# Kernel tuning notes

Hardware: AMD Instinct MI355X
Metric: run time of the kernel (lower is better)

## Reference

```python
import jax, jax.numpy as jnp
import numpy as np

B, S, L, H, N_ITEMS = 16, 20, 64, 768, 50000  # sessions, max items/session, tokens/item, hidden, catalog
T = S * L
TEMP = 0.05       # config.temp
PAD_POS = 50      # pad item position id (see torch code)
EPS = 1e-8        # torch CosineSimilarity eps


def setup_inputs() -> dict:
    key = jax.random.key(0)
    k1, k2, k3, k4 = jax.random.split(key, 4)
    hidden = jax.random.normal(k1, (B, T, H), jnp.float32)
    emb = jax.random.normal(k2, (N_ITEMS, H), jnp.float32)
    # item position ids: each item's L tokens share position 1..S; padded items -> 50
    pos = np.tile(np.repeat(np.arange(1, S + 1), L)[None, :], (B, 1))  # [B,T]
    sess_len = np.asarray(jax.random.randint(k3, (B,), S // 2, S + 1))  # items per session
    item_idx = np.repeat(np.arange(S), L)[None, :]                      # [1,T]
    pos = np.where(item_idx < sess_len[:, None], pos, PAD_POS).astype(np.int32)
    attn = (pos != PAD_POS).astype(np.int32)
    attrs = np.asarray(jax.random.randint(k4, (B, T), 0, 4)).astype(np.int32)
    return {
        "hidden_states": hidden,
        "item_embedding": emb,
        "attention_mask": jnp.asarray(attn),
        "item_position_ids": jnp.asarray(pos),
        "attr_type_ids": jnp.asarray(attrs),
    }


def reference(hidden_states, item_embedding, attention_mask, item_position_ids, attr_type_ids):
    # --- RecformerPooler (pooler_type='item'): nan-mean pool tokens per item ---
    item_ids = jnp.arange(1, S + 1, dtype=item_position_ids.dtype)
    mask = item_position_ids[:, None, :] == item_ids[None, :, None]      # [B,S,T]
    counts = mask.sum(-1)                                                # [B,S]
    valid = counts > 0                                                   # items present in session
    maskf = mask.astype(hidden_states.dtype)
    pooled = jnp.einsum('bst,bth->bsh', maskf, hidden_states)
    pooled = pooled / jnp.maximum(counts, 1)[..., None].astype(hidden_states.dtype)
    # (torch produces NaN rows for invalid items; we carry `valid` instead)

    # --- Similarity: cosine / temp vs full item catalog ---
    pn = jnp.maximum(jnp.linalg.norm(pooled, axis=-1, keepdims=True), EPS)
    en = jnp.maximum(jnp.linalg.norm(item_embedding, axis=-1, keepdims=True), EPS)
    sim = jnp.einsum('bsh,nh->bns', pooled / pn, item_embedding / en) / TEMP  # [B,N,S]

    # --- reduce_session('maxsim'): NaN -> -inf, max over session items ---
    sim = jnp.where(valid[:, None, :], sim, -jnp.inf)
    scores = sim.max(axis=-1)  # [B, N]; trailing mean over attr dim (size 1) is identity
    return scores
```

## Files before the change

### kernel.cpp

```cpp
#include <hip/hip_runtime.h>

#define B_ 16
#define S_ 20
#define L_ 64
#define T_ 1280
#define H_ 768
#define NITEMS 50000
#define TEMP 0.05f
#define EPSN 1e-8f

#define MT 80
#define ROWPAD 776
#define NKT 24

typedef __attribute__((ext_vector_type(8))) short short8;
typedef __attribute__((ext_vector_type(4))) short short4v;
typedef __attribute__((ext_vector_type(4))) float f32x4;
typedef __attribute__((ext_vector_type(4))) unsigned int u32x4;

__device__ __forceinline__ unsigned short f2bf(float f) {
    unsigned int u = __float_as_uint(f);
    u = u + 0x7FFFu + ((u >> 16) & 1u);
    return (unsigned short)(u >> 16);
}

__device__ __forceinline__ unsigned int pack_bf16(float f0, float f1) {
    const unsigned int u0 = __float_as_uint(f0) + 0x8000u;
    const unsigned int u1 = __float_as_uint(f1) + 0x8000u;
    return __builtin_amdgcn_perm(u1, u0, 0x07060302u);
}

__global__ __launch_bounds__(192) void pool_kernel(const float* __restrict__ hidden,
                                                   const int* __restrict__ pos,
                                                   unsigned short* __restrict__ A,
                                                   int* __restrict__ valid) {
    const int row = blockIdx.x;
    const int b = row / S_, s = row % S_;
    const int tid = threadIdx.x;

    __shared__ float wgt[L_];
    __shared__ int cntS;
    __shared__ float red[3];

    const int* pbase = pos + b * T_ + s * L_;
    if (tid < L_) {
        const int match = (pbase[tid] == s + 1) ? 1 : 0;
        unsigned long long bal = __ballot(match);
        wgt[tid] = match ? 1.0f : 0.0f;
        if (tid == 0) cntS = (int)__popcll(bal);
    }
    __syncthreads();

    const int cnt = cntS;
    const float inv = 1.0f / (float)(cnt > 0 ? cnt : 1);
    const float* hbase = hidden + ((size_t)b * T_ + (size_t)s * L_) * H_ + tid * 4;

    float a0 = 0.f, a1 = 0.f, a2 = 0.f, a3 = 0.f;
#pragma unroll 8
    for (int t = 0; t < L_; ++t) {
        const float w = wgt[t];
        const float4 v = *reinterpret_cast<const float4*>(hbase + (size_t)t * H_);
        a0 += w * v.x; a1 += w * v.y; a2 += w * v.z; a3 += w * v.w;
    }
    a0 *= inv; a1 *= inv; a2 *= inv; a3 *= inv;

    float ss = a0 * a0 + a1 * a1 + a2 * a2 + a3 * a3;
#pragma unroll
    for (int off = 32; off; off >>= 1) ss += __shfl_xor(ss, off, 64);
    const int wave = tid >> 6, lane = tid & 63;
    if (lane == 0) red[wave] = ss;
    __syncthreads();
    const float tot = red[0] + red[1] + red[2];
    const float scale = 1.0f / (fmaxf(sqrtf(tot), EPSN) * TEMP);

    short4v w4;
    w4[0] = (short)f2bf(a0 * scale);
    w4[1] = (short)f2bf(a1 * scale);
    w4[2] = (short)f2bf(a2 * scale);
    w4[3] = (short)f2bf(a3 * scale);
    *reinterpret_cast<short4v*>(A + (size_t)row * H_ + tid * 4) = w4;
    if (tid == 0) valid[row] = (cnt > 0) ? 1 : 0;
}

__global__ __launch_bounds__(512, 2) void gemm_kernel(const float* __restrict__ emb,
                                                      const unsigned short* __restrict__ A,
                                                      const int* __restrict__ valid,
                                                      float* __restrict__ out) {
    const int mt = blockIdx.x;
    const int nt = blockIdx.y;
    const int tid = threadIdx.x;
    const int wave = tid >> 6, lane = tid & 63, quad = lane >> 4, lq = lane & 15;

    __shared__ alignas(16) short As[MT * ROWPAD];
    __shared__ int sMask[4];

    if (tid < 4) {
        int m = 0;
        for (int s = 0; s < S_; ++s) m |= (valid[(mt * 4 + tid) * S_ + s] ? 1 : 0) << s;
        sMask[tid] = m;
    }

    const unsigned short* Ab = A + (size_t)(mt * MT) * H_;
#pragma unroll
    for (int i = 0; i < 15; ++i) {
        const int c = i * 512 + tid;
        const int r = c / 96, cc = c % 96;
        const u32x4 v = *reinterpret_cast<const u32x4*>(Ab + r * H_ + cc * 8);
        *reinterpret_cast<u32x4*>(reinterpret_cast<char*>(As) + r * (ROWPAD * 2) + cc * 16) = v;
    }
    __syncthreads();

    const int n0w = nt * 256 + wave * 32;
    int r0 = n0w + lq;        if (r0 > NITEMS - 1) r0 = NITEMS - 1;
    int r1 = n0w + 16 + lq;   if (r1 > NITEMS - 1) r1 = NITEMS - 1;
    const float* bp0 = emb + (size_t)r0 * H_ + quad * 8;
    const float* bp1 = emb + (size_t)r1 * H_ + quad * 8;

    const short* aBase[5];
#pragma unroll
    for (int mf = 0; mf < 5; ++mf)
        aBase[mf] = &As[(mf * 16 + lq) * ROWPAD + quad * 8];

    float rowSq0 = 0.f, rowSq1 = 0.f;
    f32x4 acc[5][2];
#pragma unroll
    for (int i = 0; i < 5; ++i) {
        acc[i][0] = (f32x4)0.f;
        acc[i][1] = (f32x4)0.f;
    }

#pragma unroll 8
    for (int kt = 0; kt < NKT; ++kt) {
        const float4 x0 = *reinterpret_cast<const float4*>(bp0 + kt * 32);
        const float4 y0 = *reinterpret_cast<const float4*>(bp0 + kt * 32 + 4);
        const float4 x1 = *reinterpret_cast<const float4*>(bp1 + kt * 32);
        const float4 y1 = *reinterpret_cast<const float4*>(bp1 + kt * 32 + 4);

        rowSq0 += x0.x * x0.x + x0.y * x0.y + x0.z * x0.z + x0.w * x0.w
                + y0.x * y0.x + y0.y * y0.y + y0.z * y0.z + y0.w * y0.w;
        rowSq1 += x1.x * x1.x + x1.y * x1.y + x1.z * x1.z + x1.w * x1.w
                + y1.x * y1.x + y1.y * y1.y + y1.z * y1.z + y1.w * y1.w;

        union { short8 s; u32x4 u; } bF0, bF1;
        bF0.u[0] = pack_bf16(x0.x, x0.y); bF0.u[1] = pack_bf16(x0.z, x0.w);
        bF0.u[2] = pack_bf16(y0.x, y0.y); bF0.u[3] = pack_bf16(y0.z, y0.w);
        bF1.u[0] = pack_bf16(x1.x, x1.y); bF1.u[1] = pack_bf16(x1.z, x1.w);
        bF1.u[2] = pack_bf16(y1.x, y1.y); bF1.u[3] = pack_bf16(y1.z, y1.w);

#pragma unroll
        for (int mf = 0; mf < 5; ++mf) {
            const short8 aF = *reinterpret_cast<const short8*>(aBase[mf] + kt * 32);
            acc[mf][0] = __builtin_amdgcn_mfma_f32_16x16x32_bf16(aF, bF0.s, acc[mf][0], 0, 0, 0);
            acc[mf][1] = __builtin_amdgcn_mfma_f32_16x16x32_bf16(aF, bF1.s, acc[mf][1], 0, 0, 0);
        }
    }

    rowSq0 += __shfl_xor(rowSq0, 16, 64);
    rowSq0 += __shfl_xor(rowSq0, 32, 64);
    rowSq1 += __shfl_xor(rowSq1, 16, 64);
    rowSq1 += __shfl_xor(rowSq1, 32, 64);
    float invEn[2];
    invEn[0] = 1.0f / fmaxf(sqrtf(rowSq0), EPSN);
    invEn[1] = 1.0f / fmaxf(sqrtf(rowSq1), EPSN);

#pragma unroll
    for (int nf = 0; nf < 2; ++nf) {
        const int n = n0w + nf * 16 + lq;
        const float inv_en = invEn[nf];
#pragma unroll
        for (int bb = 0; bb < 4; ++bb) {
            const int rLo = bb * S_;
            const int msk = sMask[bb];
            const int mfLo = rLo >> 4;
            const int mfHi = (rLo + S_ - 1) >> 4;
            float lm = -__builtin_inff();
#pragma unroll
            for (int mf = mfLo; mf <= mfHi; ++mf)
#pragma unroll
                for (int e = 0; e < 4; ++e) {
                    const int r = mf * 16 + quad * 4 + e;
                    const unsigned off = (unsigned)(r - rLo);
                    const bool ok = (off < (unsigned)S_) && ((msk >> off) & 1);
                    lm = ok ? fmaxf(lm, acc[mf][nf][e]) : lm;
                }
            lm = fmaxf(lm, __shfl_xor(lm, 16, 64));
            lm = fmaxf(lm, __shfl_xor(lm, 32, 64));
            if (quad == 0 && n < NITEMS)
                out[(size_t)(mt * 4 + bb) * NITEMS + n] = lm * inv_en;
        }
    }
}

extern "C" void kernel_launch(void* const* d_in, const int* in_sizes, int n_in,
                              void* d_out, int out_size, void* d_ws, size_t ws_size,
                              hipStream_t stream) {
    const float* hidden = (const float*)d_in[0];
    const float* emb    = (const float*)d_in[1];
    const int*   pos    = (const int*)d_in[3];
    float* out = (float*)d_out;

    unsigned short* Abf = (unsigned short*)d_ws;
    int* valid = (int*)((char*)d_ws + (size_t)320 * 768 * 2);

    pool_kernel<<<dim3(320), dim3(192), 0, stream>>>(hidden, pos, Abf, valid);
    gemm_kernel<<<dim3(4, 196), dim3(512), 0, stream>>>(emb, Abf, valid, out);
}
```

Before: 344.4 us.

## Drop LDS staging of A, register double-buffer loads, remap grid for L2 reuse

The GEMM kernel no longer copies the 80-row bf16 A tile into shared memory. Each wave now loads its A fragments straight from global memory (L2) into registers, double-buffered with the embedding loads so the next k-step's data is fetched while the current MFMAs run. Blocks shrink to 256 threads covering 128 catalog rows, and a 1-D grid with a swizzled block-to-tile mapping places the four M-tiles that share an embedding slice next to each other, so that slice is reused from L2. This removes the LDS fill and its barrier and allows more blocks per CU. In exchange, A traffic moves to global/L2, and the extra prefetch registers raise register pressure.

```diff
diff --git a/kernel.cpp b/kernel.cpp
--- a/kernel.cpp
+++ b/kernel.cpp
@@ -10,13 +10,13 @@
 #define EPSN 1e-8f
 
 #define MT 80
-#define ROWPAD 776
 #define NKT 24
 
 typedef __attribute__((ext_vector_type(8))) short short8;
 typedef __attribute__((ext_vector_type(4))) short short4v;
 typedef __attribute__((ext_vector_type(4))) float f32x4;
-typedef __attribute__((ext_vector_type(4))) unsigned int u32x4;
+
+union U16x4 { uint4 u; short8 s; };
 
 __device__ __forceinline__ unsigned short f2bf(float f) {
     unsigned int u = __float_as_uint(f);
@@ -82,44 +82,47 @@
     if (tid == 0) valid[row] = (cnt > 0) ? 1 : 0;
 }
 
-__global__ __launch_bounds__(512, 2) void gemm_kernel(const float* __restrict__ emb,
+__global__ __launch_bounds__(256, 3) void gemm_kernel(const float* __restrict__ emb,
                                                       const unsigned short* __restrict__ A,
                                                       const int* __restrict__ valid,
                                                       float* __restrict__ out) {
-    const int mt = blockIdx.x;
-    const int nt = blockIdx.y;
+    const int bid = blockIdx.x;
+    const int ring = bid >> 3, l8 = bid & 7;
+    const int nt = (ring >> 2) * 8 + l8;
+    const int mt = ring & 3;
     const int tid = threadIdx.x;
     const int wave = tid >> 6, lane = tid & 63, quad = lane >> 4, lq = lane & 15;
 
-    __shared__ alignas(16) short As[MT * ROWPAD];
     __shared__ int sMask[4];
-
     if (tid < 4) {
         int m = 0;
         for (int s = 0; s < S_; ++s) m |= (valid[(mt * 4 + tid) * S_ + s] ? 1 : 0) << s;
         sMask[tid] = m;
     }
-
-    const unsigned short* Ab = A + (size_t)(mt * MT) * H_;
-#pragma unroll
-    for (int i = 0; i < 15; ++i) {
-        const int c = i * 512 + tid;
-        const int r = c / 96, cc = c % 96;
-        const u32x4 v = *reinterpret_cast<const u32x4*>(Ab + r * H_ + cc * 8);
-        *reinterpret_cast<u32x4*>(reinterpret_cast<char*>(As) + r * (ROWPAD * 2) + cc * 16) = v;
-    }
     __syncthreads();
 
-    const int n0w = nt * 256 + wave * 32;
-    int r0 = n0w + lq;        if (r0 > NITEMS - 1) r0 = NITEMS - 1;
-    int r1 = n0w + 16 + lq;   if (r1 > NITEMS - 1) r1 = NITEMS - 1;
+    const int n0w = nt * 128 + wave * 32;
+    int r0 = n0w + lq;       if (r0 > NITEMS - 1) r0 = NITEMS - 1;
+    int r1 = n0w + 16 + lq;  if (r1 > NITEMS - 1) r1 = NITEMS - 1;
     const float* bp0 = emb + (size_t)r0 * H_ + quad * 8;
     const float* bp1 = emb + (size_t)r1 * H_ + quad * 8;
-
-    const short* aBase[5];
-#pragma unroll
-    for (int mf = 0; mf < 5; ++mf)
-        aBase[mf] = &As[(mf * 16 + lq) * ROWPAD + quad * 8];
+    const unsigned short* ap = A + (size_t)(mt * MT + lq) * H_ + quad * 8;
+
+    uint4 aP[2][5];
+    float4 bP[2][4];
+
+#define PREFETCH(kt, slot)                                                        \
+    do {                                                                          \
+        const int ko = (kt) * 32;                                                 \
+        _Pragma("unroll") for (int mf = 0; mf < 5; ++mf)                          \
+            aP[slot][mf] = *reinterpret_cast<const uint4*>(ap + mf * 16 * H_ + ko); \
+        bP[slot][0] = *reinterpret_cast<const float4*>(bp0 + ko);                 \
+        bP[slot][1] = *reinterpret_cast<const float4*>(bp0 + ko + 4);             \
+        bP[slot][2] = *reinterpret_cast<const float4*>(bp1 + ko);                 \
+        bP[slot][3] = *reinterpret_cast<const float4*>(bp1 + ko + 4);             \
+    } while (0)
+
+    PREFETCH(0, 0);
 
     float rowSq0 = 0.f, rowSq1 = 0.f;
     f32x4 acc[5][2];
@@ -129,31 +132,33 @@
         acc[i][1] = (f32x4)0.f;
     }
 
-#pragma unroll 8
+#pragma unroll 2
     for (int kt = 0; kt < NKT; ++kt) {
-        const float4 x0 = *reinterpret_cast<const float4*>(bp0 + kt * 32);
-        const float4 y0 = *reinterpret_cast<const float4*>(bp0 + kt * 32 + 4);
-        const float4 x1 = *reinterpret_cast<const float4*>(bp1 + kt * 32);
-        const float4 y1 = *reinterpret_cast<const float4*>(bp1 + kt * 32 + 4);
+        const int cur = kt & 1;
+        if (kt + 1 < NKT) PREFETCH(kt + 1, cur ^ 1);
+
+        const float4 x0 = bP[cur][0], y0 = bP[cur][1];
+        const float4 x1 = bP[cur][2], y1 = bP[cur][3];
 
         rowSq0 += x0.x * x0.x + x0.y * x0.y + x0.z * x0.z + x0.w * x0.w
                 + y0.x * y0.x + y0.y * y0.y + y0.z * y0.z + y0.w * y0.w;
         rowSq1 += x1.x * x1.x + x1.y * x1.y + x1.z * x1.z + x1.w * x1.w
                 + y1.x * y1.x + y1.y * y1.y + y1.z * y1.z + y1.w * y1.w;
 
-        union { short8 s; u32x4 u; } bF0, bF1;
-        bF0.u[0] = pack_bf16(x0.x, x0.y); bF0.u[1] = pack_bf16(x0.z, x0.w);
-        bF0.u[2] = pack_bf16(y0.x, y0.y); bF0.u[3] = pack_bf16(y0.z, y0.w);
-        bF1.u[0] = pack_bf16(x1.x, x1.y); bF1.u[1] = pack_bf16(x1.z, x1.w);
-        bF1.u[2] = pack_bf16(y1.x, y1.y); bF1.u[3] = pack_bf16(y1.z, y1.w);
+        U16x4 bF0, bF1;
+        bF0.u.x = pack_bf16(x0.x, x0.y); bF0.u.y = pack_bf16(x0.z, x0.w);
+        bF0.u.z = pack_bf16(y0.x, y0.y); bF0.u.w = pack_bf16(y0.z, y0.w);
+        bF1.u.x = pack_bf16(x1.x, x1.y); bF1.u.y = pack_bf16(x1.z, x1.w);
+        bF1.u.z = pack_bf16(y1.x, y1.y); bF1.u.w = pack_bf16(y1.z, y1.w);
 
 #pragma unroll
         for (int mf = 0; mf < 5; ++mf) {
-            const short8 aF = *reinterpret_cast<const short8*>(aBase[mf] + kt * 32);
-            acc[mf][0] = __builtin_amdgcn_mfma_f32_16x16x32_bf16(aF, bF0.s, acc[mf][0], 0, 0, 0);
-            acc[mf][1] = __builtin_amdgcn_mfma_f32_16x16x32_bf16(aF, bF1.s, acc[mf][1], 0, 0, 0);
+            U16x4 aF; aF.u = aP[cur][mf];
+            acc[mf][0] = __builtin_amdgcn_mfma_f32_16x16x32_bf16(aF.s, bF0.s, acc[mf][0], 0, 0, 0);
+            acc[mf][1] = __builtin_amdgcn_mfma_f32_16x16x32_bf16(aF.s, bF1.s, acc[mf][1], 0, 0, 0);
         }
     }
+#undef PREFETCH
 
     rowSq0 += __shfl_xor(rowSq0, 16, 64);
     rowSq0 += __shfl_xor(rowSq0, 32, 64);
@@ -203,5 +208,5 @@
     int* valid = (int*)((char*)d_ws + (size_t)320 * 768 * 2);
 
     pool_kernel<<<dim3(320), dim3(192), 0, stream>>>(hidden, pos, Abf, valid);
-    gemm_kernel<<<dim3(4, 196), dim3(512), 0, stream>>>(emb, Abf, valid, out);
-}
+    gemm_kernel<<<dim3(1568), dim3(256), 0, stream>>>(emb, Abf, valid, out);
+}
```

Result: slower. 384.0 us (+11.5%).

## Restructure GEMM so each block reads embedding once and streams packed A

Applied to the files above, without the earlier changes.

The grid changes from (4 M-tiles x 196 N-tiles) to a 1D grid over 48-item N tiles. Each block stages its embedding rows in LDS as bf16 once and covers all 320 pooled rows across 4 waves. The old layout read every embedding row four times from global memory; the new one reads it once. The pool kernel now writes A in an MFMA-fragment-packed layout that is read directly from global/L2 with a 3-deep register prefetch, and embedding norms are computed from the bf16 LDS copy. The costs are heavier per-block LDS staging with no overlap against compute, and norms are now taken from bf16-rounded values.

```diff
diff --git a/kernel.cpp b/kernel.cpp
--- a/kernel.cpp
+++ b/kernel.cpp
@@ -9,14 +9,15 @@
 #define TEMP 0.05f
 #define EPSN 1e-8f
 
-#define MT 80
-#define ROWPAD 776
+#define BN 48
+#define RSTRIDE 776
 #define NKT 24
 
 typedef __attribute__((ext_vector_type(8))) short short8;
 typedef __attribute__((ext_vector_type(4))) short short4v;
 typedef __attribute__((ext_vector_type(4))) float f32x4;
-typedef __attribute__((ext_vector_type(4))) unsigned int u32x4;
+
+union U16x4 { uint4 u; short8 s; };
 
 __device__ __forceinline__ unsigned short f2bf(float f) {
     unsigned int u = __float_as_uint(f);
@@ -30,12 +31,17 @@
     return __builtin_amdgcn_perm(u1, u0, 0x07060302u);
 }
 
+__device__ __forceinline__ float bf2f(unsigned short u) {
+    return __uint_as_float(((unsigned int)u) << 16);
+}
+
 __global__ __launch_bounds__(192) void pool_kernel(const float* __restrict__ hidden,
                                                    const int* __restrict__ pos,
-                                                   unsigned short* __restrict__ A,
+                                                   unsigned short* __restrict__ Apack,
                                                    int* __restrict__ valid) {
     const int row = blockIdx.x;
     const int b = row / S_, s = row % S_;
+    const int r16 = row >> 4, lqr = row & 15;
     const int tid = threadIdx.x;
 
     __shared__ float wgt[L_];
@@ -67,110 +73,123 @@
     float ss = a0 * a0 + a1 * a1 + a2 * a2 + a3 * a3;
 #pragma unroll
     for (int off = 32; off; off >>= 1) ss += __shfl_xor(ss, off, 64);
-    const int wave = tid >> 6, lane = tid & 63;
-    if (lane == 0) red[wave] = ss;
+    const int wv = tid >> 6, lane = tid & 63;
+    if (lane == 0) red[wv] = ss;
     __syncthreads();
     const float tot = red[0] + red[1] + red[2];
     const float scale = 1.0f / (fmaxf(sqrtf(tot), EPSN) * TEMP);
 
+    const int kt = tid >> 3, quad = (tid >> 1) & 3, j0 = (tid & 1) * 4;
     short4v w4;
     w4[0] = (short)f2bf(a0 * scale);
     w4[1] = (short)f2bf(a1 * scale);
     w4[2] = (short)f2bf(a2 * scale);
     w4[3] = (short)f2bf(a3 * scale);
-    *reinterpret_cast<short4v*>(A + (size_t)row * H_ + tid * 4) = w4;
+    *reinterpret_cast<short4v*>(Apack + ((size_t)r16 * NKT + kt) * 512 +
+                                (quad * 16 + lqr) * 8 + j0) = w4;
     if (tid == 0) valid[row] = (cnt > 0) ? 1 : 0;
 }
 
-__global__ __launch_bounds__(512, 2) void gemm_kernel(const float* __restrict__ emb,
-                                                      const unsigned short* __restrict__ A,
+__global__ __launch_bounds__(256, 2) void gemm_kernel(const float* __restrict__ emb,
+                                                      const unsigned short* __restrict__ Apack,
                                                       const int* __restrict__ valid,
                                                       float* __restrict__ out) {
-    const int mt = blockIdx.x;
-    const int nt = blockIdx.y;
+    const int nt = blockIdx.x;
+    const int n0 = nt * BN;
     const int tid = threadIdx.x;
     const int wave = tid >> 6, lane = tid & 63, quad = lane >> 4, lq = lane & 15;
 
-    __shared__ alignas(16) short As[MT * ROWPAD];
-    __shared__ int sMask[4];
-
-    if (tid < 4) {
+    __shared__ alignas(16) short Bs[BN * RSTRIDE];
+    __shared__ float sInvEn[BN];
+    __shared__ int sMask[B_];
+
+    if (tid < B_) {
         int m = 0;
-        for (int s = 0; s < S_; ++s) m |= (valid[(mt * 4 + tid) * S_ + s] ? 1 : 0) << s;
+        for (int s = 0; s < S_; ++s) m |= (valid[tid * S_ + s] ? 1 : 0) << s;
         sMask[tid] = m;
     }
 
-    const unsigned short* Ab = A + (size_t)(mt * MT) * H_;
-#pragma unroll
-    for (int i = 0; i < 15; ++i) {
-        const int c = i * 512 + tid;
-        const int r = c / 96, cc = c % 96;
-        const u32x4 v = *reinterpret_cast<const u32x4*>(Ab + r * H_ + cc * 8);
-        *reinterpret_cast<u32x4*>(reinterpret_cast<char*>(As) + r * (ROWPAD * 2) + cc * 16) = v;
-    }
-    __syncthreads();
-
-    const int n0w = nt * 256 + wave * 32;
-    int r0 = n0w + lq;        if (r0 > NITEMS - 1) r0 = NITEMS - 1;
-    int r1 = n0w + 16 + lq;   if (r1 > NITEMS - 1) r1 = NITEMS - 1;
-    const float* bp0 = emb + (size_t)r0 * H_ + quad * 8;
-    const float* bp1 = emb + (size_t)r1 * H_ + quad * 8;
-
-    const short* aBase[5];
+#pragma unroll
+    for (int i = 0; i < 36; ++i) {
+        const int f = i * 256 + tid;
+        const int row = (unsigned)f / 192u;
+        const int c4 = f - row * 192;
+        int gr = n0 + row; if (gr > NITEMS - 1) gr = NITEMS - 1;
+        const float4 v = *reinterpret_cast<const float4*>(emb + (size_t)gr * H_ + c4 * 4);
+        uint2 w;
+        w.x = pack_bf16(v.x, v.y);
+        w.y = pack_bf16(v.z, v.w);
+        *reinterpret_cast<uint2*>(reinterpret_cast<char*>(Bs) + row * (RSTRIDE * 2) + c4 * 8) = w;
+    }
+    __syncthreads();
+
+    if (tid < 192) {
+        const int row = tid >> 2, sub = tid & 3;
+        const char* rp = reinterpret_cast<const char*>(Bs) + row * (RSTRIDE * 2) + sub * 384;
+        float ss = 0.f;
+#pragma unroll
+        for (int i = 0; i < 24; ++i) {
+            const short8 v = *reinterpret_cast<const short8*>(rp + i * 16);
+#pragma unroll
+            for (int j = 0; j < 8; ++j) {
+                const float x = bf2f((unsigned short)v[j]);
+                ss += x * x;
+            }
+        }
+        ss += __shfl_xor(ss, 1, 64);
+        ss += __shfl_xor(ss, 2, 64);
+        if (sub == 0) sInvEn[row] = 1.0f / fmaxf(sqrtf(ss), EPSN);
+    }
+    __syncthreads();
+
+    const unsigned short* apf[5];
 #pragma unroll
     for (int mf = 0; mf < 5; ++mf)
-        aBase[mf] = &As[(mf * 16 + lq) * ROWPAD + quad * 8];
-
-    float rowSq0 = 0.f, rowSq1 = 0.f;
-    f32x4 acc[5][2];
-#pragma unroll
-    for (int i = 0; i < 5; ++i) {
-        acc[i][0] = (f32x4)0.f;
-        acc[i][1] = (f32x4)0.f;
-    }
-
-#pragma unroll 8
+        apf[mf] = Apack + ((size_t)(wave * 5 + mf) * NKT) * 512 + lane * 8;
+    const char* bb = reinterpret_cast<const char*>(Bs) + lq * (RSTRIDE * 2) + quad * 16;
+
+    U16x4 aP[3][5];
+    short8 bP[2][3];
+    f32x4 acc[5][3];
+#pragma unroll
+    for (int mf = 0; mf < 5; ++mf)
+#pragma unroll
+        for (int g = 0; g < 3; ++g) acc[mf][g] = (f32x4)0.f;
+
+#define LOADA(kt, slot)                                                           \
+    _Pragma("unroll") for (int mf = 0; mf < 5; ++mf)                              \
+        aP[slot][mf].u = *reinterpret_cast<const uint4*>(apf[mf] + (kt) * 512)
+#define LOADB(kt, slot)                                                           \
+    _Pragma("unroll") for (int g = 0; g < 3; ++g)                                 \
+        bP[slot][g] = *reinterpret_cast<const short8*>(bb + g * 16 * (RSTRIDE * 2) + (kt) * 64)
+
+    LOADA(0, 0);
+    LOADA(1, 1);
+    LOADB(0, 0);
+
+#pragma unroll
     for (int kt = 0; kt < NKT; ++kt) {
-        const float4 x0 = *reinterpret_cast<const float4*>(bp0 + kt * 32);
-        const float4 y0 = *reinterpret_cast<const float4*>(bp0 + kt * 32 + 4);
-        const float4 x1 = *reinterpret_cast<const float4*>(bp1 + kt * 32);
-        const float4 y1 = *reinterpret_cast<const float4*>(bp1 + kt * 32 + 4);
-
-        rowSq0 += x0.x * x0.x + x0.y * x0.y + x0.z * x0.z + x0.w * x0.w
-                + y0.x * y0.x + y0.y * y0.y + y0.z * y0.z + y0.w * y0.w;
-        rowSq1 += x1.x * x1.x + x1.y * x1.y + x1.z * x1.z + x1.w * x1.w
-                + y1.x * y1.x + y1.y * y1.y + y1.z * y1.z + y1.w * y1.w;
-
-        union { short8 s; u32x4 u; } bF0, bF1;
-        bF0.u[0] = pack_bf16(x0.x, x0.y); bF0.u[1] = pack_bf16(x0.z, x0.w);
-        bF0.u[2] = pack_bf16(y0.x, y0.y); bF0.u[3] = pack_bf16(y0.z, y0.w);
-        bF1.u[0] = pack_bf16(x1.x, x1.y); bF1.u[1] = pack_bf16(x1.z, x1.w);
-        bF1.u[2] = pack_bf16(y1.x, y1.y); bF1.u[3] = pack_bf16(y1.z, y1.w);
-
-#pragma unroll
-        for (int mf = 0; mf < 5; ++mf) {
-            const short8 aF = *reinterpret_cast<const short8*>(aBase[mf] + kt * 32);
-            acc[mf][0] = __builtin_amdgcn_mfma_f32_16x16x32_bf16(aF, bF0.s, acc[mf][0], 0, 0, 0);
-            acc[mf][1] = __builtin_amdgcn_mfma_f32_16x16x32_bf16(aF, bF1.s, acc[mf][1], 0, 0, 0);
-        }
-    }
-
-    rowSq0 += __shfl_xor(rowSq0, 16, 64);
-    rowSq0 += __shfl_xor(rowSq0, 32, 64);
-    rowSq1 += __shfl_xor(rowSq1, 16, 64);
-    rowSq1 += __shfl_xor(rowSq1, 32, 64);
-    float invEn[2];
-    invEn[0] = 1.0f / fmaxf(sqrtf(rowSq0), EPSN);
-    invEn[1] = 1.0f / fmaxf(sqrtf(rowSq1), EPSN);
-
-#pragma unroll
-    for (int nf = 0; nf < 2; ++nf) {
-        const int n = n0w + nf * 16 + lq;
-        const float inv_en = invEn[nf];
-#pragma unroll
-        for (int bb = 0; bb < 4; ++bb) {
-            const int rLo = bb * S_;
-            const int msk = sMask[bb];
+        if (kt + 2 < NKT) { LOADA(kt + 2, (kt + 2) % 3); }
+        if (kt + 1 < NKT) { LOADB(kt + 1, (kt + 1) & 1); }
+#pragma unroll
+        for (int mf = 0; mf < 5; ++mf)
+#pragma unroll
+            for (int g = 0; g < 3; ++g)
+                acc[mf][g] = __builtin_amdgcn_mfma_f32_16x16x32_bf16(
+                    aP[kt % 3][mf].s, bP[kt & 1][g], acc[mf][g], 0, 0, 0);
+    }
+#undef LOADA
+#undef LOADB
+
+#pragma unroll
+    for (int g = 0; g < 3; ++g) {
+        const int ncol = g * 16 + lq;
+        const int n = n0 + ncol;
+        const float inv_en = sInvEn[ncol];
+#pragma unroll
+        for (int bb4 = 0; bb4 < 4; ++bb4) {
+            const int rLo = bb4 * S_;
+            const int msk = sMask[wave * 4 + bb4];
             const int mfLo = rLo >> 4;
             const int mfHi = (rLo + S_ - 1) >> 4;
             float lm = -__builtin_inff();
@@ -181,12 +200,12 @@
                     const int r = mf * 16 + quad * 4 + e;
                     const unsigned off = (unsigned)(r - rLo);
                     const bool ok = (off < (unsigned)S_) && ((msk >> off) & 1);
-                    lm = ok ? fmaxf(lm, acc[mf][nf][e]) : lm;
+                    lm = ok ? fmaxf(lm, acc[mf][g][e]) : lm;
                 }
             lm = fmaxf(lm, __shfl_xor(lm, 16, 64));
             lm = fmaxf(lm, __shfl_xor(lm, 32, 64));
             if (quad == 0 && n < NITEMS)
-                out[(size_t)(mt * 4 + bb) * NITEMS + n] = lm * inv_en;
+                out[(size_t)(wave * 4 + bb4) * NITEMS + n] = lm * inv_en;
         }
     }
 }
@@ -199,9 +218,9 @@
     const int*   pos    = (const int*)d_in[3];
     float* out = (float*)d_out;
 
-    unsigned short* Abf = (unsigned short*)d_ws;
-    int* valid = (int*)((char*)d_ws + (size_t)320 * 768 * 2);
-
-    pool_kernel<<<dim3(320), dim3(192), 0, stream>>>(hidden, pos, Abf, valid);
-    gemm_kernel<<<dim3(4, 196), dim3(512), 0, stream>>>(emb, Abf, valid, out);
-}
+    unsigned short* Apack = (unsigned short*)d_ws;
+    int* valid = (int*)((char*)d_ws + (size_t)20 * NKT * 512 * 2);
+
+    pool_kernel<<<dim3(320), dim3(192), 0, stream>>>(hidden, pos, Apack, valid);
+    gemm_kernel<<<dim3((NITEMS + BN - 1) / BN), dim3(256), 0, stream>>>(emb, Apack, valid, out);
+}
```

Result: faster. 312.1 us (-9.4%).
